# Kernel tuning notes

Hardware: AMD Instinct MI355X
Metric: run time of the kernel (lower is better)

## Reference

```python
import jax, jax.numpy as jnp
import numpy as np

VOCAB, EMB, SEQ = 10000, 256, 250
BATCH, UNITS = 256, 1024


def setup_inputs() -> dict:
    key = jax.random.key(0)
    ks = jax.random.split(key, 12)
    s = lambda k, shape, scale: jax.random.normal(k, shape, dtype=jnp.float32) * scale
    return {
        "tokens": jax.random.randint(ks[0], (BATCH, SEQ), 0, VOCAB),
        "emb": s(ks[1], (VOCAB, EMB), 1.0),
        "W1": s(ks[2], (EMB, 2 * UNITS), 1.0 / np.sqrt(EMB)),
        "b1": jnp.zeros((2 * UNITS,), jnp.float32),
        "W2": s(ks[3], (2 * UNITS, UNITS), 1.0 / np.sqrt(2 * UNITS)),
        "b2": jnp.zeros((UNITS,), jnp.float32),
        "W3": s(ks[4], (EMB, UNITS), 1.0 / np.sqrt(EMB)),
        "b3": jnp.zeros((UNITS,), jnp.float32),
        "W4": s(ks[5], (EMB, UNITS), 1.0 / np.sqrt(EMB)),
        "b4": jnp.zeros((UNITS,), jnp.float32),
        "W5": s(ks[6], (EMB, UNITS), 1.0 / np.sqrt(EMB)),
        "Wout": s(ks[7], (UNITS, 1), 1.0 / np.sqrt(UNITS)),
        "bout": jnp.zeros((1,), jnp.float32),
        "state0": s(ks[8], (BATCH, UNITS), 1.0),
    }


def reference(tokens, emb, W1, b1, W2, b2, W3, b3, W4, b4, W5, Wout, bout, state0):
    x = emb[tokens]  # [B, T, E]

    def cell(s, x_t):
        r = jax.nn.relu(x_t @ W1 + b1)          # [B, 2U]
        m = jnp.tanh(r @ W2 + b2)               # [B, U]
        forget = m * s
        i = jax.nn.sigmoid(x_t @ W3 + b3)
        g = jnp.tanh(x_t @ W4 + b4)
        y = jax.nn.relu(forget + i * g)
        s_new = jax.nn.relu(jax.nn.relu(x_t @ W5) + y)
        return s_new, None

    s_final, _ = jax.lax.scan(cell, state0, jnp.swapaxes(x, 0, 1))  # scan over T
    return jax.nn.sigmoid(s_final @ Wout + bout)  # [B, 1]
```

## Files before the change

kernel.cpp:

```cpp
#include <hip/hip_runtime.h>
#include <math.h>

typedef _Float16 f16;
typedef _Float16 f16x2 __attribute__((ext_vector_type(2)));
typedef _Float16 f16x4 __attribute__((ext_vector_type(4)));
typedef _Float16 f16x8 __attribute__((ext_vector_type(8)));
typedef float f32x4 __attribute__((ext_vector_type(4)));

#define AS1 __attribute__((address_space(1)))
#define AS3 __attribute__((address_space(3)))

__device__ __forceinline__ void gload_lds16(const void* g, void* l) {
    __builtin_amdgcn_global_load_lds((AS1 void*)(g), (AS3 void*)(l), 16, 0, 0);
}

__device__ __forceinline__ float sigmoid_fast(float v) {
    return __builtin_amdgcn_rcpf(1.f + __builtin_amdgcn_exp2f(-1.44269504f * v));
}
__device__ __forceinline__ float tanh_fast(float v) {
    return 1.f - 2.f * __builtin_amdgcn_rcpf(1.f + __builtin_amdgcn_exp2f(2.88539008f * v));
}

__global__ __launch_bounds__(256) void tpose_kernel(const float* __restrict__ W, f16* __restrict__ Wt,
                                                    int K, int N) {
    __shared__ float T[64][65];
    const int k0 = blockIdx.x * 64, n0 = blockIdx.y * 64;
    const int tid = threadIdx.x;
    const int rr = tid >> 4, cc = (tid & 15) * 4;
#pragma unroll
    for (int p = 0; p < 4; ++p) {
        int k = rr + p * 16;
        float4 v = *(const float4*)&W[(size_t)(k0 + k) * N + n0 + cc];
        T[k][cc] = v.x; T[k][cc + 1] = v.y; T[k][cc + 2] = v.z; T[k][cc + 3] = v.w;
    }
    __syncthreads();
#pragma unroll
    for (int p = 0; p < 4; ++p) {
        int n = rr + p * 16;
        f16x4 h;
        h[0] = (f16)T[cc][n]; h[1] = (f16)T[cc + 1][n];
        h[2] = (f16)T[cc + 2][n]; h[3] = (f16)T[cc + 3][n];
        *(f16x4*)&Wt[(size_t)(n0 + n) * K + k0 + cc] = h;
    }
}

__global__ __launch_bounds__(256) void ecast_kernel(const float* __restrict__ emb, f16* __restrict__ E) {
    int r = blockIdx.x * 4 + (threadIdx.x >> 6);
    int c = (threadIdx.x & 63) * 4;
    float4 v = make_float4(0.f, 0.f, 0.f, 0.f);
    if (r < 10000) v = *(const float4*)&emb[(size_t)r * 256 + c];
    f16x4 h;
    h[0] = (f16)v.x; h[1] = (f16)v.y; h[2] = (f16)v.z; h[3] = (f16)v.w;
    *(f16x4*)&E[(size_t)r * 256 + c] = h;
}

template <int MODE>
__global__ __launch_bounds__(512, 4) void gemm_main(
    const f16* __restrict__ A, const f16* __restrict__ Bt, int N, int K, int CT,
    const float* __restrict__ bb1, const float* __restrict__ bb3, const float* __restrict__ bb4,
    f16* __restrict__ O0, f16* __restrict__ O1, f16* __restrict__ O3) {
    constexpr int BN    = (MODE == 0) ? 256 : 128;
    constexpr int BK    = (MODE == 0) ? 32 : 64;
    constexpr int NF    = BN / 64;
    constexpr int WNOFF = BN / 4;
    constexpr int SLOTS = BK / 8, SMASK = SLOTS - 1;
    constexpr int LOG2S = (BK == 32) ? 2 : 3;
    constexpr int RSH   = (BK == 32) ? 1 : 0;
    constexpr int ABUF  = 160 * BK;
    constexpr int BBUF  = BN * BK;
    constexpr int BUFSZ = ABUF + BBUF;
    constexpr int ACH   = 160 * SLOTS;
    constexpr int BCH   = BN * SLOTS;
    constexpr int AIT   = (ACH + 511) / 512;
    constexpr int BIT   = BCH / 512;
    constexpr int SMSZ  = (MODE == 0) ? 40960 : 36864;
    __shared__ __align__(16) f16 SM[SMSZ];
    f16* Cs = SM;
    const int nwg = gridDim.x, orig = blockIdx.x;
    const int q = nwg >> 3, rm = nwg & 7;
    const int xcd = orig & 7, loc = orig >> 3;
    const int wg = (xcd < rm ? xcd * (q + 1) : rm * (q + 1) + (xcd - rm) * q) + loc;
    const int rowT = wg / CT, colT = wg - rowT * CT;
    const int row0 = rowT * 160, col0 = colT * BN;

    const int tid = threadIdx.x;
    const int wave = tid >> 6, lane = tid & 63;
    const int wr = wave >> 2, wc = wave & 3;
    const int lo16 = lane & 15, hi4 = lane >> 4;

    const bool PM = (MODE == 0) && (col0 >= 2048) && (col0 < 4096);

    f32x4 acc[5][NF] = {};

    const f16* aptr[AIT]; int adst[AIT];
    const f16* bptr[BIT]; int bdst[BIT];
#pragma unroll
    for (int it = 0; it < AIT; ++it) {
        int c = it * 512 + tid;
        int r = c >> LOG2S, sl = c & SMASK;
        int kc = (sl ^ ((r >> RSH) & SMASK)) << 3;
        aptr[it] = A + (size_t)(row0 + (r < 160 ? r : 0)) * K + kc;
        adst[it] = c * 8;
    }
#pragma unroll
    for (int it = 0; it < BIT; ++it) {
        int c = it * 512 + tid;
        int r = c >> LOG2S, sl = c & SMASK;
        int kc = (sl ^ ((r >> RSH) & SMASK)) << 3;
        int brow = col0 + r;
        if (PM) {
            int qc = col0 - 2048 + r;
            int grp = qc >> 5, q2 = qc & 31;
            brow = (q2 < 16) ? (2048 + grp * 16 + q2) : (3072 + grp * 16 + (q2 - 16));
        }
        bptr[it] = Bt + (size_t)brow * K + kc;
        bdst[it] = c * 8;
    }

    auto stage = [&](int buf, int k0) {
        f16* As = SM + buf * BUFSZ;
        f16* Bs = As + ABUF;
#pragma unroll
        for (int it = 0; it < AIT; ++it)
            if ((it + 1) * 512 <= ACH || tid < ACH - it * 512)
                gload_lds16(aptr[it] + k0, &As[adst[it]]);
#pragma unroll
        for (int it = 0; it < BIT; ++it)
            gload_lds16(bptr[it] + k0, &Bs[bdst[it]]);
    };

    const int nt = K / BK;
    stage(0, 0);
    __syncthreads();
    for (int t = 0; t < nt; ++t) {
        if (t + 1 < nt) stage((t + 1) & 1, (t + 1) * BK);
        const f16* As = SM + (t & 1) * BUFSZ;
        const f16* Bs = As + ABUF;
#pragma unroll
        for (int kk = 0; kk < BK; kk += 32) {
            const int s0 = (kk >> 3) + hi4;
            f16x8 af[5], bf[NF];
#pragma unroll
            for (int m = 0; m < 5; ++m) {
                int row = wr * 80 + m * 16 + lo16;
                af[m] = *(const f16x8*)&As[row * BK + ((s0 ^ ((row >> RSH) & SMASK)) << 3)];
            }
#pragma unroll
            for (int n = 0; n < NF; ++n) {
                int row = wc * WNOFF + n * 16 + lo16;
                bf[n] = *(const f16x8*)&Bs[row * BK + ((s0 ^ ((row >> RSH) & SMASK)) << 3)];
            }
#pragma unroll
            for (int m = 0; m < 5; ++m)
#pragma unroll
                for (int n = 0; n < NF; ++n)
                    acc[m][n] = __builtin_amdgcn_mfma_f32_16x16x32_f16(af[m], bf[n], acc[m][n], 0, 0, 0);
        }
        __syncthreads();
    }

    if (MODE == 1) {
        const float* bp = bb1 + col0;
#pragma unroll
        for (int n = 0; n < 2; ++n) {
            int col = wc * 32 + n * 16 + lo16;
            float b = bp[col];
            int ch = col >> 3, el = col & 7;
#pragma unroll
            for (int m = 0; m < 5; ++m)
#pragma unroll
                for (int j = 0; j < 4; ++j) {
                    int row = wr * 80 + m * 16 + hi4 * 4 + j;
                    Cs[row * 128 + ((ch ^ (row & 15)) << 3) + el] = (f16)tanh_fast(acc[m][n][j] + b);
                }
        }
        __syncthreads();
#pragma unroll
        for (int it = 0; it < 5; ++it) {
            int idx = it * 512 + tid;
            int row = idx >> 4, ch = idx & 15;
            f16x8 v = *(const f16x8*)&Cs[row * 128 + ((ch ^ (row & 15)) << 3)];
            *(f16x8*)&O0[(size_t)(row0 + row) * 1024 + col0 + ch * 8] = v;
        }
        return;
    }

    if (PM) {
        const int pcol0 = (col0 - 2048) >> 1;
#pragma unroll
        for (int p = 0; p < 2; ++p) {
            int colP = wc * 32 + p * 16 + lo16;
            float bi = bb3[pcol0 + colP], bg = bb4[pcol0 + colP];
            int ch = colP >> 3, el = colP & 7;
#pragma unroll
            for (int m = 0; m < 5; ++m)
#pragma unroll
                for (int j = 0; j < 4; ++j) {
                    int row = wr * 80 + m * 16 + hi4 * 4 + j;
                    float pi = sigmoid_fast(acc[m][2 * p][j] + bi);
                    float pg = tanh_fast(acc[m][2 * p + 1][j] + bg);
                    Cs[row * 128 + ((ch ^ (row & 15)) << 3) + el] = (f16)(pi * pg);
                }
        }
        __syncthreads();
#pragma unroll
        for (int it = 0; it < 5; ++it) {
            int idx = it * 512 + tid;
            int row = idx >> 4, ch = idx & 15;
            f16x8 v = *(const f16x8*)&Cs[row * 128 + ((ch ^ (row & 15)) << 3)];
            *(f16x8*)&O1[(size_t)(row0 + row) * 1024 + pcol0 + ch * 8] = v;
        }
        return;
    }

    f16* Oe; size_t ostr; const float* bp;
    if (col0 < 2048) { Oe = O0 + col0;          ostr = 2048; bp = bb1 + col0; }
    else             { Oe = O3 + (col0 - 4096); ostr = 1024; bp = nullptr;    }

#pragma unroll
    for (int n = 0; n < NF; ++n) {
        int col = wc * WNOFF + n * 16 + lo16;
        float b = bp ? bp[col] : 0.f;
        int ch = col >> 3, el = col & 7;
#pragma unroll
        for (int m = 0; m < 5; ++m)
#pragma unroll
            for (int j = 0; j < 4; ++j) {
                int row = wr * 80 + m * 16 + hi4 * 4 + j;
                Cs[row * 256 + ((ch ^ (row & 31)) << 3) + el] = (f16)fmaxf(acc[m][n][j] + b, 0.f);
            }
    }
    __syncthreads();

#pragma unroll
    for (int it = 0; it < 10; ++it) {
        int idx = it * 512 + tid;
        int row = idx >> 5, ch = idx & 31;
        f16x8 v = *(const f16x8*)&Cs[row * 256 + ((ch ^ (row & 31)) << 3)];
        *(f16x8*)&Oe[(size_t)(row0 + row) * ostr + ch * 8] = v;
    }
}

__global__ __launch_bounds__(64) void scan_slice_kernel(
    const int* __restrict__ tokens, const f16* __restrict__ Mt, const f16* __restrict__ Pt,
    const f16* __restrict__ Ut, const float* __restrict__ state0,
    const float* __restrict__ Wout, float* __restrict__ partial) {
    __shared__ int toks[288];
    const int bid = blockIdx.x;
    const int b = bid >> 3, x = bid & 7;
    const int lane = threadIdx.x;
    for (int t = lane; t < 288; t += 64) toks[t] = (t < 250) ? tokens[b * 250 + t] : 0;
    __syncthreads();

    const int u0 = x * 128 + lane * 2;
    float2 sv = *(const float2*)&state0[(size_t)b * 1024 + u0];
    float s0 = sv.x, s1 = sv.y;

    f16x2 m[32], p[32], u[32];
#pragma unroll
    for (int k = 0; k < 20; ++k) {
        size_t nb = (size_t)toks[k] * 1024 + u0;
        m[k] = *(const f16x2*)&Mt[nb];
        p[k] = *(const f16x2*)&Pt[nb];
        u[k] = *(const f16x2*)&Ut[nb];
    }

    for (int tb = 0; tb < 224; tb += 32) {
#pragma unroll
        for (int k = 0; k < 32; ++k) {
            const int ls = (k + 20) & 31;
            size_t nb = (size_t)toks[tb + k + 20] * 1024 + u0;
            m[ls] = *(const f16x2*)&Mt[nb];
            p[ls] = *(const f16x2*)&Pt[nb];
            u[ls] = *(const f16x2*)&Ut[nb];
            float y0 = fmaxf((float)m[k][0] * s0 + (float)p[k][0], 0.f);
            s0 = fmaxf((float)u[k][0] + y0, 0.f);
            float y1 = fmaxf((float)m[k][1] * s1 + (float)p[k][1], 0.f);
            s1 = fmaxf((float)u[k][1] + y1, 0.f);
        }
    }
#pragma unroll
    for (int k = 0; k < 26; ++k) {
        if (k < 6) {
            const int ls = k + 20;
            size_t nb = (size_t)toks[244 + k] * 1024 + u0;
            m[ls] = *(const f16x2*)&Mt[nb];
            p[ls] = *(const f16x2*)&Pt[nb];
            u[ls] = *(const f16x2*)&Ut[nb];
        }
        float y0 = fmaxf((float)m[k][0] * s0 + (float)p[k][0], 0.f);
        s0 = fmaxf((float)u[k][0] + y0, 0.f);
        float y1 = fmaxf((float)m[k][1] * s1 + (float)p[k][1], 0.f);
        s1 = fmaxf((float)u[k][1] + y1, 0.f);
    }

    float2 wv = *(const float2*)&Wout[u0];
    float part = s0 * wv.x + s1 * wv.y;
#pragma unroll
    for (int o = 32; o > 0; o >>= 1) part += __shfl_down(part, o, 64);
    if (lane == 0) partial[bid] = part;
}

__global__ __launch_bounds__(256) void final_kernel(const float* __restrict__ partial,
                                                    const float* __restrict__ bout,
                                                    float* __restrict__ out) {
    int b = threadIdx.x;
    float tot = bout[0];
#pragma unroll
    for (int w = 0; w < 8; ++w) tot += partial[b * 8 + w];
    out[b] = sigmoid_fast(tot);
}

extern "C" void kernel_launch(void* const* d_in, const int* in_sizes, int n_in,
                              void* d_out, int out_size, void* d_ws, size_t ws_size,
                              hipStream_t stream) {
    const int*   tokens = (const int*)  d_in[0];
    const float* emb    = (const float*)d_in[1];
    const float* W1     = (const float*)d_in[2];
    const float* b1     = (const float*)d_in[3];
    const float* W2     = (const float*)d_in[4];
    const float* b2     = (const float*)d_in[5];
    const float* W3     = (const float*)d_in[6];
    const float* b3     = (const float*)d_in[7];
    const float* W4     = (const float*)d_in[8];
    const float* b4     = (const float*)d_in[9];
    const float* W5     = (const float*)d_in[10];
    const float* Wout   = (const float*)d_in[11];
    const float* bout   = (const float*)d_in[12];
    const float* state0 = (const float*)d_in[13];
    float* out = (float*)d_out;

    const int RP = 10240;

    char* ws = (char*)d_ws;
    size_t off = 0;
    auto alloc = [&](size_t bytes) -> void* {
        void* p = ws + off;
        off += (bytes + 255) & ~(size_t)255;
        return p;
    };
    f16* WtQ = (f16*)alloc((size_t)5120 * 256 * 2);
    f16* Wt2 = (f16*)alloc((size_t)1024 * 2048 * 2);
    f16* E   = (f16*)alloc((size_t)RP * 256 * 2);
    f16* Rb  = (f16*)alloc((size_t)RP * 2048 * 2);
    f16* Mt  = (f16*)alloc((size_t)RP * 1024 * 2);
    f16* Pt  = (f16*)alloc((size_t)RP * 1024 * 2);
    f16* Ut  = (f16*)alloc((size_t)RP * 1024 * 2);
    float* partial = (float*)alloc((size_t)2048 * 4);
    (void)ws_size; (void)in_sizes; (void)n_in; (void)out_size;

    tpose_kernel<<<dim3(4, 32),  256, 0, stream>>>(W1, WtQ,               256, 2048);
    tpose_kernel<<<dim3(4, 16),  256, 0, stream>>>(W3, WtQ + 2048 * 256,  256, 1024);
    tpose_kernel<<<dim3(4, 16),  256, 0, stream>>>(W4, WtQ + 3072 * 256,  256, 1024);
    tpose_kernel<<<dim3(4, 16),  256, 0, stream>>>(W5, WtQ + 4096 * 256,  256, 1024);
    tpose_kernel<<<dim3(32, 16), 256, 0, stream>>>(W2, Wt2,              2048, 1024);
    ecast_kernel<<<RP / 4, 256, 0, stream>>>(emb, E);

    gemm_main<0><<<(RP / 160) * (5120 / 256), 512, 0, stream>>>(
        E, WtQ, 5120, 256, 5120 / 256, b1, b3, b4, Rb, Pt, Ut);
    gemm_main<1><<<(RP / 160) * (1024 / 128), 512, 0, stream>>>(
        Rb, Wt2, 1024, 2048, 1024 / 128, b2, nullptr, nullptr, Mt, nullptr, nullptr);

    scan_slice_kernel<<<2048, 64, 0, stream>>>(tokens, Mt, Pt, Ut, state0, Wout, partial);
    final_kernel<<<1, 256, 0, stream>>>(partial, bout, out);
}
```

Before: 155.6 us.

## Triple-buffer GEMM LDS pipeline with vmcnt waits and merge small transposes

Splits the templated GEMM into two specialized kernels that use a three-stage LDS ring with prefetch distance two. Per-wave s_waitcnt vmcnt counts combined with raw s_barrier replace the full __syncthreads after each tile, and s_setprio is raised around the MFMA block. The second GEMM drops its BK from 64 to 32 to fit the three buffers in LDS. It also merges the four small weight transposes into one launch to cut launch overhead. The hand-counted vmcnt values must match the number of loads each wave issues, or LDS reads could race with in-flight loads.

```diff
diff --git a/kernel.cpp b/kernel.cpp
--- a/kernel.cpp
+++ b/kernel.cpp
@@ -14,11 +14,45 @@
     __builtin_amdgcn_global_load_lds((AS1 void*)(g), (AS3 void*)(l), 16, 0, 0);
 }
 
+template <int N> __device__ __forceinline__ void vmwait() {
+    asm volatile("s_waitcnt vmcnt(%0)" :: "n"(N) : "memory");
+}
+
 __device__ __forceinline__ float sigmoid_fast(float v) {
     return __builtin_amdgcn_rcpf(1.f + __builtin_amdgcn_exp2f(-1.44269504f * v));
 }
 __device__ __forceinline__ float tanh_fast(float v) {
     return 1.f - 2.f * __builtin_amdgcn_rcpf(1.f + __builtin_amdgcn_exp2f(2.88539008f * v));
+}
+
+__global__ __launch_bounds__(256) void tposeq_kernel(
+    const float* __restrict__ W1, const float* __restrict__ W3,
+    const float* __restrict__ W4, const float* __restrict__ W5, f16* __restrict__ Wt) {
+    __shared__ float T[64][65];
+    const int y = blockIdx.y;
+    const float* W; int nw, n0, orow;
+    if (y < 32)      { W = W1; nw = 2048; n0 = y * 64;        orow = 0;    }
+    else if (y < 48) { W = W3; nw = 1024; n0 = (y - 32) * 64; orow = 2048; }
+    else if (y < 64) { W = W4; nw = 1024; n0 = (y - 48) * 64; orow = 3072; }
+    else             { W = W5; nw = 1024; n0 = (y - 64) * 64; orow = 4096; }
+    const int k0 = blockIdx.x * 64;
+    const int tid = threadIdx.x;
+    const int rr = tid >> 4, cc = (tid & 15) * 4;
+#pragma unroll
+    for (int p = 0; p < 4; ++p) {
+        int k = rr + p * 16;
+        float4 v = *(const float4*)&W[(size_t)(k0 + k) * nw + n0 + cc];
+        T[k][cc] = v.x; T[k][cc + 1] = v.y; T[k][cc + 2] = v.z; T[k][cc + 3] = v.w;
+    }
+    __syncthreads();
+#pragma unroll
+    for (int p = 0; p < 4; ++p) {
+        int n = rr + p * 16;
+        f16x4 h;
+        h[0] = (f16)T[cc][n]; h[1] = (f16)T[cc + 1][n];
+        h[2] = (f16)T[cc + 2][n]; h[3] = (f16)T[cc + 3][n];
+        *(f16x4*)&Wt[(size_t)(orow + n0 + n) * 256 + k0 + cc] = h;
+    }
 }
 
 __global__ __launch_bounds__(256) void tpose_kernel(const float* __restrict__ W, f16* __restrict__ Wt,
@@ -54,58 +88,46 @@
     *(f16x4*)&E[(size_t)r * 256 + c] = h;
 }
 
-template <int MODE>
-__global__ __launch_bounds__(512, 4) void gemm_main(
-    const f16* __restrict__ A, const f16* __restrict__ Bt, int N, int K, int CT,
+__global__ __launch_bounds__(512, 4) void gemm0_kernel(
+    const f16* __restrict__ A, const f16* __restrict__ Bt,
     const float* __restrict__ bb1, const float* __restrict__ bb3, const float* __restrict__ bb4,
     f16* __restrict__ O0, f16* __restrict__ O1, f16* __restrict__ O3) {
-    constexpr int BN    = (MODE == 0) ? 256 : 128;
-    constexpr int BK    = (MODE == 0) ? 32 : 64;
-    constexpr int NF    = BN / 64;
-    constexpr int WNOFF = BN / 4;
-    constexpr int SLOTS = BK / 8, SMASK = SLOTS - 1;
-    constexpr int LOG2S = (BK == 32) ? 2 : 3;
-    constexpr int RSH   = (BK == 32) ? 1 : 0;
-    constexpr int ABUF  = 160 * BK;
-    constexpr int BBUF  = BN * BK;
-    constexpr int BUFSZ = ABUF + BBUF;
-    constexpr int ACH   = 160 * SLOTS;
-    constexpr int BCH   = BN * SLOTS;
-    constexpr int AIT   = (ACH + 511) / 512;
-    constexpr int BIT   = BCH / 512;
-    constexpr int SMSZ  = (MODE == 0) ? 40960 : 36864;
-    __shared__ __align__(16) f16 SM[SMSZ];
+    constexpr int BK = 32, SMASK = 3, RSH = 1;
+    constexpr int ABUF = 160 * BK, BBUF = 256 * BK, BUFSZ = ABUF + BBUF;
+    constexpr int CT = 20;
+    __shared__ __align__(16) f16 SM[40960];
     f16* Cs = SM;
     const int nwg = gridDim.x, orig = blockIdx.x;
     const int q = nwg >> 3, rm = nwg & 7;
     const int xcd = orig & 7, loc = orig >> 3;
     const int wg = (xcd < rm ? xcd * (q + 1) : rm * (q + 1) + (xcd - rm) * q) + loc;
     const int rowT = wg / CT, colT = wg - rowT * CT;
-    const int row0 = rowT * 160, col0 = colT * BN;
+    const int row0 = rowT * 160, col0 = colT * 256;
 
     const int tid = threadIdx.x;
     const int wave = tid >> 6, lane = tid & 63;
     const int wr = wave >> 2, wc = wave & 3;
     const int lo16 = lane & 15, hi4 = lane >> 4;
-
-    const bool PM = (MODE == 0) && (col0 >= 2048) && (col0 < 4096);
-
-    f32x4 acc[5][NF] = {};
-
-    const f16* aptr[AIT]; int adst[AIT];
-    const f16* bptr[BIT]; int bdst[BIT];
-#pragma unroll
-    for (int it = 0; it < AIT; ++it) {
+    const bool hv = (wave < 2);
+
+    const bool PM = (col0 >= 2048) && (col0 < 4096);
+
+    f32x4 acc[5][4] = {};
+
+    const f16* aptr[2]; int adst[2];
+    const f16* bptr[2]; int bdst[2];
+#pragma unroll
+    for (int it = 0; it < 2; ++it) {
         int c = it * 512 + tid;
-        int r = c >> LOG2S, sl = c & SMASK;
+        int r = c >> 2, sl = c & 3;
         int kc = (sl ^ ((r >> RSH) & SMASK)) << 3;
-        aptr[it] = A + (size_t)(row0 + (r < 160 ? r : 0)) * K + kc;
+        aptr[it] = A + (size_t)(row0 + (r < 160 ? r : 0)) * 256 + kc;
         adst[it] = c * 8;
     }
 #pragma unroll
-    for (int it = 0; it < BIT; ++it) {
+    for (int it = 0; it < 2; ++it) {
         int c = it * 512 + tid;
-        int r = c >> LOG2S, sl = c & SMASK;
+        int r = c >> 2, sl = c & 3;
         int kc = (sl ^ ((r >> RSH) & SMASK)) << 3;
         int brow = col0 + r;
         if (PM) {
@@ -113,76 +135,54 @@
             int grp = qc >> 5, q2 = qc & 31;
             brow = (q2 < 16) ? (2048 + grp * 16 + q2) : (3072 + grp * 16 + (q2 - 16));
         }
-        bptr[it] = Bt + (size_t)brow * K + kc;
+        bptr[it] = Bt + (size_t)brow * 256 + kc;
         bdst[it] = c * 8;
     }
 
     auto stage = [&](int buf, int k0) {
         f16* As = SM + buf * BUFSZ;
         f16* Bs = As + ABUF;
-#pragma unroll
-        for (int it = 0; it < AIT; ++it)
-            if ((it + 1) * 512 <= ACH || tid < ACH - it * 512)
-                gload_lds16(aptr[it] + k0, &As[adst[it]]);
-#pragma unroll
-        for (int it = 0; it < BIT; ++it)
-            gload_lds16(bptr[it] + k0, &Bs[bdst[it]]);
+        gload_lds16(aptr[0] + k0, &As[adst[0]]);
+        if (tid < 128) gload_lds16(aptr[1] + k0, &As[adst[1]]);
+        gload_lds16(bptr[0] + k0, &Bs[bdst[0]]);
+        gload_lds16(bptr[1] + k0, &Bs[bdst[1]]);
     };
 
-    const int nt = K / BK;
     stage(0, 0);
-    __syncthreads();
-    for (int t = 0; t < nt; ++t) {
-        if (t + 1 < nt) stage((t + 1) & 1, (t + 1) * BK);
-        const f16* As = SM + (t & 1) * BUFSZ;
+    stage(1, 32);
+    if (hv) vmwait<4>(); else vmwait<3>();
+    __builtin_amdgcn_s_barrier();
+
+    int rbuf = 0, sbuf = 2;
+    for (int t = 0; t < 8; ++t) {
+        if (t + 2 < 8) stage(sbuf, (t + 2) * 32);
+        const f16* As = SM + rbuf * BUFSZ;
         const f16* Bs = As + ABUF;
-#pragma unroll
-        for (int kk = 0; kk < BK; kk += 32) {
-            const int s0 = (kk >> 3) + hi4;
-            f16x8 af[5], bf[NF];
-#pragma unroll
-            for (int m = 0; m < 5; ++m) {
-                int row = wr * 80 + m * 16 + lo16;
-                af[m] = *(const f16x8*)&As[row * BK + ((s0 ^ ((row >> RSH) & SMASK)) << 3)];
-            }
-#pragma unroll
-            for (int n = 0; n < NF; ++n) {
-                int row = wc * WNOFF + n * 16 + lo16;
-                bf[n] = *(const f16x8*)&Bs[row * BK + ((s0 ^ ((row >> RSH) & SMASK)) << 3)];
-            }
-#pragma unroll
-            for (int m = 0; m < 5; ++m)
-#pragma unroll
-                for (int n = 0; n < NF; ++n)
-                    acc[m][n] = __builtin_amdgcn_mfma_f32_16x16x32_f16(af[m], bf[n], acc[m][n], 0, 0, 0);
-        }
-        __syncthreads();
-    }
-
-    if (MODE == 1) {
-        const float* bp = bb1 + col0;
-#pragma unroll
-        for (int n = 0; n < 2; ++n) {
-            int col = wc * 32 + n * 16 + lo16;
-            float b = bp[col];
-            int ch = col >> 3, el = col & 7;
-#pragma unroll
-            for (int m = 0; m < 5; ++m)
-#pragma unroll
-                for (int j = 0; j < 4; ++j) {
-                    int row = wr * 80 + m * 16 + hi4 * 4 + j;
-                    Cs[row * 128 + ((ch ^ (row & 15)) << 3) + el] = (f16)tanh_fast(acc[m][n][j] + b);
-                }
-        }
-        __syncthreads();
-#pragma unroll
-        for (int it = 0; it < 5; ++it) {
-            int idx = it * 512 + tid;
-            int row = idx >> 4, ch = idx & 15;
-            f16x8 v = *(const f16x8*)&Cs[row * 128 + ((ch ^ (row & 15)) << 3)];
-            *(f16x8*)&O0[(size_t)(row0 + row) * 1024 + col0 + ch * 8] = v;
-        }
-        return;
+        f16x8 af[5], bf[4];
+#pragma unroll
+        for (int m = 0; m < 5; ++m) {
+            int row = wr * 80 + m * 16 + lo16;
+            af[m] = *(const f16x8*)&As[row * BK + ((hi4 ^ ((row >> RSH) & SMASK)) << 3)];
+        }
+#pragma unroll
+        for (int n = 0; n < 4; ++n) {
+            int row = wc * 64 + n * 16 + lo16;
+            bf[n] = *(const f16x8*)&Bs[row * BK + ((hi4 ^ ((row >> RSH) & SMASK)) << 3)];
+        }
+        __builtin_amdgcn_s_setprio(1);
+#pragma unroll
+        for (int m = 0; m < 5; ++m)
+#pragma unroll
+            for (int n = 0; n < 4; ++n)
+                acc[m][n] = __builtin_amdgcn_mfma_f32_16x16x32_f16(af[m], bf[n], acc[m][n], 0, 0, 0);
+        __builtin_amdgcn_s_setprio(0);
+        if (t + 1 < 8) {
+            if (t + 2 < 8) { if (hv) vmwait<4>(); else vmwait<3>(); }
+            else vmwait<0>();
+        }
+        __builtin_amdgcn_s_barrier();
+        rbuf = (rbuf == 2) ? 0 : rbuf + 1;
+        sbuf = (sbuf == 2) ? 0 : sbuf + 1;
     }
 
     if (PM) {
@@ -218,8 +218,8 @@
     else             { Oe = O3 + (col0 - 4096); ostr = 1024; bp = nullptr;    }
 
 #pragma unroll
-    for (int n = 0; n < NF; ++n) {
-        int col = wc * WNOFF + n * 16 + lo16;
+    for (int n = 0; n < 4; ++n) {
+        int col = wc * 64 + n * 16 + lo16;
         float b = bp ? bp[col] : 0.f;
         int ch = col >> 3, el = col & 7;
 #pragma unroll
@@ -231,13 +231,122 @@
             }
     }
     __syncthreads();
-
 #pragma unroll
     for (int it = 0; it < 10; ++it) {
         int idx = it * 512 + tid;
         int row = idx >> 5, ch = idx & 31;
         f16x8 v = *(const f16x8*)&Cs[row * 256 + ((ch ^ (row & 31)) << 3)];
         *(f16x8*)&Oe[(size_t)(row0 + row) * ostr + ch * 8] = v;
+    }
+}
+
+__global__ __launch_bounds__(512, 4) void gemm1_kernel(
+    const f16* __restrict__ A, const f16* __restrict__ Bt,
+    const float* __restrict__ bb2, f16* __restrict__ O0) {
+    constexpr int BK = 32, SMASK = 3, RSH = 1;
+    constexpr int ABUF = 160 * BK, BBUF = 128 * BK, BUFSZ = ABUF + BBUF;
+    constexpr int CT = 8;
+    __shared__ __align__(16) f16 SM[27648];
+    f16* Cs = SM;
+    const int nwg = gridDim.x, orig = blockIdx.x;
+    const int q = nwg >> 3, rm = nwg & 7;
+    const int xcd = orig & 7, loc = orig >> 3;
+    const int wg = (xcd < rm ? xcd * (q + 1) : rm * (q + 1) + (xcd - rm) * q) + loc;
+    const int rowT = wg / CT, colT = wg - rowT * CT;
+    const int row0 = rowT * 160, col0 = colT * 128;
+
+    const int tid = threadIdx.x;
+    const int wave = tid >> 6, lane = tid & 63;
+    const int wr = wave >> 2, wc = wave & 3;
+    const int lo16 = lane & 15, hi4 = lane >> 4;
+    const bool hv = (wave < 2);
+
+    f32x4 acc[5][2] = {};
+
+    const f16* aptr[2]; int adst[2];
+    const f16* bptr0; int bdst0;
+#pragma unroll
+    for (int it = 0; it < 2; ++it) {
+        int c = it * 512 + tid;
+        int r = c >> 2, sl = c & 3;
+        int kc = (sl ^ ((r >> RSH) & SMASK)) << 3;
+        aptr[it] = A + (size_t)(row0 + (r < 160 ? r : 0)) * 2048 + kc;
+        adst[it] = c * 8;
+    }
+    {
+        int c = tid;
+        int r = c >> 2, sl = c & 3;
+        int kc = (sl ^ ((r >> RSH) & SMASK)) << 3;
+        bptr0 = Bt + (size_t)(col0 + r) * 2048 + kc;
+        bdst0 = c * 8;
+    }
+
+    auto stage = [&](int buf, int k0) {
+        f16* As = SM + buf * BUFSZ;
+        f16* Bs = As + ABUF;
+        gload_lds16(aptr[0] + k0, &As[adst[0]]);
+        if (tid < 128) gload_lds16(aptr[1] + k0, &As[adst[1]]);
+        gload_lds16(bptr0 + k0, &Bs[bdst0]);
+    };
+
+    stage(0, 0);
+    stage(1, 32);
+    if (hv) vmwait<3>(); else vmwait<2>();
+    __builtin_amdgcn_s_barrier();
+
+    int rbuf = 0, sbuf = 2;
+    for (int t = 0; t < 64; ++t) {
+        if (t + 2 < 64) stage(sbuf, (t + 2) * 32);
+        const f16* As = SM + rbuf * BUFSZ;
+        const f16* Bs = As + ABUF;
+        f16x8 af[5], bf[2];
+#pragma unroll
+        for (int m = 0; m < 5; ++m) {
+            int row = wr * 80 + m * 16 + lo16;
+            af[m] = *(const f16x8*)&As[row * BK + ((hi4 ^ ((row >> RSH) & SMASK)) << 3)];
+        }
+#pragma unroll
+        for (int n = 0; n < 2; ++n) {
+            int row = wc * 32 + n * 16 + lo16;
+            bf[n] = *(const f16x8*)&Bs[row * BK + ((hi4 ^ ((row >> RSH) & SMASK)) << 3)];
+        }
+        __builtin_amdgcn_s_setprio(1);
+#pragma unroll
+        for (int m = 0; m < 5; ++m)
+#pragma unroll
+            for (int n = 0; n < 2; ++n)
+                acc[m][n] = __builtin_amdgcn_mfma_f32_16x16x32_f16(af[m], bf[n], acc[m][n], 0, 0, 0);
+        __builtin_amdgcn_s_setprio(0);
+        if (t + 1 < 64) {
+            if (t + 2 < 64) { if (hv) vmwait<3>(); else vmwait<2>(); }
+            else vmwait<0>();
+        }
+        __builtin_amdgcn_s_barrier();
+        rbuf = (rbuf == 2) ? 0 : rbuf + 1;
+        sbuf = (sbuf == 2) ? 0 : sbuf + 1;
+    }
+
+    const float* bp = bb2 + col0;
+#pragma unroll
+    for (int n = 0; n < 2; ++n) {
+        int col = wc * 32 + n * 16 + lo16;
+        float b = bp[col];
+        int ch = col >> 3, el = col & 7;
+#pragma unroll
+        for (int m = 0; m < 5; ++m)
+#pragma unroll
+            for (int j = 0; j < 4; ++j) {
+                int row = wr * 80 + m * 16 + hi4 * 4 + j;
+                Cs[row * 128 + ((ch ^ (row & 15)) << 3) + el] = (f16)tanh_fast(acc[m][n][j] + b);
+            }
+    }
+    __syncthreads();
+#pragma unroll
+    for (int it = 0; it < 5; ++it) {
+        int idx = it * 512 + tid;
+        int row = idx >> 4, ch = idx & 15;
+        f16x8 v = *(const f16x8*)&Cs[row * 128 + ((ch ^ (row & 15)) << 3)];
+        *(f16x8*)&O0[(size_t)(row0 + row) * 1024 + col0 + ch * 8] = v;
     }
 }
 
@@ -349,17 +458,14 @@
     float* partial = (float*)alloc((size_t)2048 * 4);
     (void)ws_size; (void)in_sizes; (void)n_in; (void)out_size;
 
-    tpose_kernel<<<dim3(4, 32),  256, 0, stream>>>(W1, WtQ,               256, 2048);
-    tpose_kernel<<<dim3(4, 16),  256, 0, stream>>>(W3, WtQ + 2048 * 256,  256, 1024);
-    tpose_kernel<<<dim3(4, 16),  256, 0, stream>>>(W4, WtQ + 3072 * 256,  256, 1024);
-    tpose_kernel<<<dim3(4, 16),  256, 0, stream>>>(W5, WtQ + 4096 * 256,  256, 1024);
-    tpose_kernel<<<dim3(32, 16), 256, 0, stream>>>(W2, Wt2,              2048, 1024);
+    tposeq_kernel<<<dim3(4, 80), 256, 0, stream>>>(W1, W3, W4, W5, WtQ);
+    tpose_kernel<<<dim3(32, 16), 256, 0, stream>>>(W2, Wt2, 2048, 1024);
     ecast_kernel<<<RP / 4, 256, 0, stream>>>(emb, E);
 
-    gemm_main<0><<<(RP / 160) * (5120 / 256), 512, 0, stream>>>(
-        E, WtQ, 5120, 256, 5120 / 256, b1, b3, b4, Rb, Pt, Ut);
-    gemm_main<1><<<(RP / 160) * (1024 / 128), 512, 0, stream>>>(
-        Rb, Wt2, 1024, 2048, 1024 / 128, b2, nullptr, nullptr, Mt, nullptr, nullptr);
+    gemm0_kernel<<<(RP / 160) * (5120 / 256), 512, 0, stream>>>(
+        E, WtQ, b1, b3, b4, Rb, Pt, Ut);
+    gemm1_kernel<<<(RP / 160) * (1024 / 128), 512, 0, stream>>>(
+        Rb, Wt2, b2, Mt);
 
     scan_slice_kernel<<<2048, 64, 0, stream>>>(tokens, Mt, Pt, Ut, state0, Wout, partial);
     final_kernel<<<1, 256, 0, stream>>>(partial, bout, out);
```

New measurement: 163.0 us. 4.8% more time.

## Shrink GEMM LDS footprint for higher occupancy and merge weight transposes

Applied to the files above, without the earlier changes.

Four transpose launches for W1/W3/W4/W5 are folded into one kernel indexed by blockIdx.y, which saves launch overhead. The GEMM now uses BK=32 for both modes and writes the MODE 0 epilogue through a 128-column staging buffer in two passes. Together these cut shared memory per block (40960→26624 and 36864→20480 halves), and launch bounds rise to 6 blocks per CU to exploit that. The cost is more K iterations and barriers in the mode-1 GEMM, an extra sync in the epilogue, and possible register pressure from the higher occupancy target.

```diff
diff --git a/kernel.cpp b/kernel.cpp
--- a/kernel.cpp
+++ b/kernel.cpp
@@ -19,6 +19,36 @@
 }
 __device__ __forceinline__ float tanh_fast(float v) {
     return 1.f - 2.f * __builtin_amdgcn_rcpf(1.f + __builtin_amdgcn_exp2f(2.88539008f * v));
+}
+
+__global__ __launch_bounds__(256) void tposeq_kernel(
+    const float* __restrict__ W1, const float* __restrict__ W3,
+    const float* __restrict__ W4, const float* __restrict__ W5, f16* __restrict__ Wt) {
+    __shared__ float T[64][65];
+    const int y = blockIdx.y;
+    const float* W; int nw, n0, orow;
+    if (y < 32)      { W = W1; nw = 2048; n0 = y * 64;        orow = 0;    }
+    else if (y < 48) { W = W3; nw = 1024; n0 = (y - 32) * 64; orow = 2048; }
+    else if (y < 64) { W = W4; nw = 1024; n0 = (y - 48) * 64; orow = 3072; }
+    else             { W = W5; nw = 1024; n0 = (y - 64) * 64; orow = 4096; }
+    const int k0 = blockIdx.x * 64;
+    const int tid = threadIdx.x;
+    const int rr = tid >> 4, cc = (tid & 15) * 4;
+#pragma unroll
+    for (int p = 0; p < 4; ++p) {
+        int k = rr + p * 16;
+        float4 v = *(const float4*)&W[(size_t)(k0 + k) * nw + n0 + cc];
+        T[k][cc] = v.x; T[k][cc + 1] = v.y; T[k][cc + 2] = v.z; T[k][cc + 3] = v.w;
+    }
+    __syncthreads();
+#pragma unroll
+    for (int p = 0; p < 4; ++p) {
+        int n = rr + p * 16;
+        f16x4 h;
+        h[0] = (f16)T[cc][n]; h[1] = (f16)T[cc + 1][n];
+        h[2] = (f16)T[cc + 2][n]; h[3] = (f16)T[cc + 3][n];
+        *(f16x4*)&Wt[(size_t)(orow + n0 + n) * 256 + k0 + cc] = h;
+    }
 }
 
 __global__ __launch_bounds__(256) void tpose_kernel(const float* __restrict__ W, f16* __restrict__ Wt,
@@ -55,25 +85,20 @@
 }
 
 template <int MODE>
-__global__ __launch_bounds__(512, 4) void gemm_main(
+__global__ __launch_bounds__(512, 6) void gemm_main(
     const f16* __restrict__ A, const f16* __restrict__ Bt, int N, int K, int CT,
     const float* __restrict__ bb1, const float* __restrict__ bb3, const float* __restrict__ bb4,
     f16* __restrict__ O0, f16* __restrict__ O1, f16* __restrict__ O3) {
     constexpr int BN    = (MODE == 0) ? 256 : 128;
-    constexpr int BK    = (MODE == 0) ? 32 : 64;
+    constexpr int BK    = 32;
     constexpr int NF    = BN / 64;
     constexpr int WNOFF = BN / 4;
-    constexpr int SLOTS = BK / 8, SMASK = SLOTS - 1;
-    constexpr int LOG2S = (BK == 32) ? 2 : 3;
-    constexpr int RSH   = (BK == 32) ? 1 : 0;
+    constexpr int SMASK = 3, RSH = 1;
     constexpr int ABUF  = 160 * BK;
     constexpr int BBUF  = BN * BK;
     constexpr int BUFSZ = ABUF + BBUF;
-    constexpr int ACH   = 160 * SLOTS;
-    constexpr int BCH   = BN * SLOTS;
-    constexpr int AIT   = (ACH + 511) / 512;
-    constexpr int BIT   = BCH / 512;
-    constexpr int SMSZ  = (MODE == 0) ? 40960 : 36864;
+    constexpr int BIT   = BN / 128;
+    constexpr int SMSZ  = (MODE == 0) ? 26624 : 20480;
     __shared__ __align__(16) f16 SM[SMSZ];
     f16* Cs = SM;
     const int nwg = gridDim.x, orig = blockIdx.x;
@@ -92,12 +117,12 @@
 
     f32x4 acc[5][NF] = {};
 
-    const f16* aptr[AIT]; int adst[AIT];
+    const f16* aptr[2]; int adst[2];
     const f16* bptr[BIT]; int bdst[BIT];
 #pragma unroll
-    for (int it = 0; it < AIT; ++it) {
+    for (int it = 0; it < 2; ++it) {
         int c = it * 512 + tid;
-        int r = c >> LOG2S, sl = c & SMASK;
+        int r = c >> 2, sl = c & 3;
         int kc = (sl ^ ((r >> RSH) & SMASK)) << 3;
         aptr[it] = A + (size_t)(row0 + (r < 160 ? r : 0)) * K + kc;
         adst[it] = c * 8;
@@ -105,7 +130,7 @@
 #pragma unroll
     for (int it = 0; it < BIT; ++it) {
         int c = it * 512 + tid;
-        int r = c >> LOG2S, sl = c & SMASK;
+        int r = c >> 2, sl = c & 3;
         int kc = (sl ^ ((r >> RSH) & SMASK)) << 3;
         int brow = col0 + r;
         if (PM) {
@@ -120,42 +145,36 @@
     auto stage = [&](int buf, int k0) {
         f16* As = SM + buf * BUFSZ;
         f16* Bs = As + ABUF;
-#pragma unroll
-        for (int it = 0; it < AIT; ++it)
-            if ((it + 1) * 512 <= ACH || tid < ACH - it * 512)
-                gload_lds16(aptr[it] + k0, &As[adst[it]]);
+        gload_lds16(aptr[0] + k0, &As[adst[0]]);
+        if (tid < 128) gload_lds16(aptr[1] + k0, &As[adst[1]]);
 #pragma unroll
         for (int it = 0; it < BIT; ++it)
             gload_lds16(bptr[it] + k0, &Bs[bdst[it]]);
     };
 
-    const int nt = K / BK;
+    const int nt = K >> 5;
     stage(0, 0);
     __syncthreads();
     for (int t = 0; t < nt; ++t) {
-        if (t + 1 < nt) stage((t + 1) & 1, (t + 1) * BK);
+        if (t + 1 < nt) stage((t + 1) & 1, (t + 1) << 5);
         const f16* As = SM + (t & 1) * BUFSZ;
         const f16* Bs = As + ABUF;
-#pragma unroll
-        for (int kk = 0; kk < BK; kk += 32) {
-            const int s0 = (kk >> 3) + hi4;
-            f16x8 af[5], bf[NF];
-#pragma unroll
-            for (int m = 0; m < 5; ++m) {
-                int row = wr * 80 + m * 16 + lo16;
-                af[m] = *(const f16x8*)&As[row * BK + ((s0 ^ ((row >> RSH) & SMASK)) << 3)];
-            }
-#pragma unroll
-            for (int n = 0; n < NF; ++n) {
-                int row = wc * WNOFF + n * 16 + lo16;
-                bf[n] = *(const f16x8*)&Bs[row * BK + ((s0 ^ ((row >> RSH) & SMASK)) << 3)];
-            }
-#pragma unroll
-            for (int m = 0; m < 5; ++m)
-#pragma unroll
-                for (int n = 0; n < NF; ++n)
-                    acc[m][n] = __builtin_amdgcn_mfma_f32_16x16x32_f16(af[m], bf[n], acc[m][n], 0, 0, 0);
-        }
+        f16x8 af[5], bf[NF];
+#pragma unroll
+        for (int m = 0; m < 5; ++m) {
+            int row = wr * 80 + m * 16 + lo16;
+            af[m] = *(const f16x8*)&As[row * BK + ((hi4 ^ ((row >> RSH) & SMASK)) << 3)];
+        }
+#pragma unroll
+        for (int n = 0; n < NF; ++n) {
+            int row = wc * WNOFF + n * 16 + lo16;
+            bf[n] = *(const f16x8*)&Bs[row * BK + ((hi4 ^ ((row >> RSH) & SMASK)) << 3)];
+        }
+#pragma unroll
+        for (int m = 0; m < 5; ++m)
+#pragma unroll
+            for (int n = 0; n < NF; ++n)
+                acc[m][n] = __builtin_amdgcn_mfma_f32_16x16x32_f16(af[m], bf[n], acc[m][n], 0, 0, 0);
         __syncthreads();
     }
 
@@ -218,26 +237,32 @@
     else             { Oe = O3 + (col0 - 4096); ostr = 1024; bp = nullptr;    }
 
 #pragma unroll
-    for (int n = 0; n < NF; ++n) {
-        int col = wc * WNOFF + n * 16 + lo16;
-        float b = bp ? bp[col] : 0.f;
-        int ch = col >> 3, el = col & 7;
-#pragma unroll
-        for (int m = 0; m < 5; ++m)
-#pragma unroll
-            for (int j = 0; j < 4; ++j) {
-                int row = wr * 80 + m * 16 + hi4 * 4 + j;
-                Cs[row * 256 + ((ch ^ (row & 31)) << 3) + el] = (f16)fmaxf(acc[m][n][j] + b, 0.f);
+    for (int pass = 0; pass < 2; ++pass) {
+        if ((wc >> 1) == pass) {
+#pragma unroll
+            for (int n = 0; n < 4; ++n) {
+                int colL = (wc & 1) * 64 + n * 16 + lo16;
+                float b = bp ? bp[pass * 128 + colL] : 0.f;
+                int ch = colL >> 3, el = colL & 7;
+#pragma unroll
+                for (int m = 0; m < 5; ++m)
+#pragma unroll
+                    for (int j = 0; j < 4; ++j) {
+                        int row = wr * 80 + m * 16 + hi4 * 4 + j;
+                        Cs[row * 128 + ((ch ^ (row & 15)) << 3) + el] =
+                            (f16)fmaxf(acc[m][n][j] + b, 0.f);
+                    }
             }
-    }
-    __syncthreads();
-
-#pragma unroll
-    for (int it = 0; it < 10; ++it) {
-        int idx = it * 512 + tid;
-        int row = idx >> 5, ch = idx & 31;
-        f16x8 v = *(const f16x8*)&Cs[row * 256 + ((ch ^ (row & 31)) << 3)];
-        *(f16x8*)&Oe[(size_t)(row0 + row) * ostr + ch * 8] = v;
+        }
+        __syncthreads();
+#pragma unroll
+        for (int it = 0; it < 5; ++it) {
+            int idx = it * 512 + tid;
+            int row = idx >> 4, ch = idx & 15;
+            f16x8 v = *(const f16x8*)&Cs[row * 128 + ((ch ^ (row & 15)) << 3)];
+            *(f16x8*)&Oe[(size_t)(row0 + row) * ostr + pass * 128 + ch * 8] = v;
+        }
+        if (pass == 0) __syncthreads();
     }
 }
 
@@ -349,11 +374,8 @@
     float* partial = (float*)alloc((size_t)2048 * 4);
     (void)ws_size; (void)in_sizes; (void)n_in; (void)out_size;
 
-    tpose_kernel<<<dim3(4, 32),  256, 0, stream>>>(W1, WtQ,               256, 2048);
-    tpose_kernel<<<dim3(4, 16),  256, 0, stream>>>(W3, WtQ + 2048 * 256,  256, 1024);
-    tpose_kernel<<<dim3(4, 16),  256, 0, stream>>>(W4, WtQ + 3072 * 256,  256, 1024);
-    tpose_kernel<<<dim3(4, 16),  256, 0, stream>>>(W5, WtQ + 4096 * 256,  256, 1024);
-    tpose_kernel<<<dim3(32, 16), 256, 0, stream>>>(W2, Wt2,              2048, 1024);
+    tposeq_kernel<<<dim3(4, 80), 256, 0, stream>>>(W1, W3, W4, W5, WtQ);
+    tpose_kernel<<<dim3(32, 16), 256, 0, stream>>>(W2, Wt2, 2048, 1024);
     ecast_kernel<<<RP / 4, 256, 0, stream>>>(emb, E);
 
     gemm_main<0><<<(RP / 160) * (5120 / 256), 512, 0, stream>>>(
```

Result: slower. 460.0 us (+195.6%).
